# Kernel tuning notes

Measured on AMD Instinct MI355X. Metric: run time of the kernel, lower is better.

Reference implementation:

```python
import jax, jax.numpy as jnp
import numpy as np

INPUT_DIM = 64
HIDDEN_DIM = 10
OUTPUT_DIM = 5
BATCH = 4096


def setup_inputs() -> dict:
    key = jax.random.key(0)
    ks = jax.random.split(key, 11)
    s = 0.1
    return {
        "x": jax.random.normal(ks[0], (BATCH, INPUT_DIM), dtype=jnp.float32),
        # phi: Linear(1, H) -> ReLU -> Linear(H, O)
        "phi_W1": jax.random.normal(ks[1], (1, HIDDEN_DIM), dtype=jnp.float32) * s,
        "phi_b1": jax.random.normal(ks[2], (HIDDEN_DIM,), dtype=jnp.float32) * s,
        "phi_W2": jax.random.normal(ks[3], (HIDDEN_DIM, OUTPUT_DIM), dtype=jnp.float32) * s,
        "phi_b2": jax.random.normal(ks[4], (OUTPUT_DIM,), dtype=jnp.float32) * s,
        # attention: Linear(O, 1)
        "attn_W": jax.random.normal(ks[5], (OUTPUT_DIM, 1), dtype=jnp.float32) * s,
        "attn_b": jax.random.normal(ks[6], (1,), dtype=jnp.float32) * s,
        # psi: Linear(2*O, H) -> ReLU -> Linear(H, O)
        "psi_W1": jax.random.normal(ks[7], (2 * OUTPUT_DIM, HIDDEN_DIM), dtype=jnp.float32) * s,
        "psi_b1": jax.random.normal(ks[8], (HIDDEN_DIM,), dtype=jnp.float32) * s,
        "psi_W2": jax.random.normal(ks[9], (HIDDEN_DIM, OUTPUT_DIM), dtype=jnp.float32) * s,
        "psi_b2": jax.random.normal(ks[10], (OUTPUT_DIM,), dtype=jnp.float32) * s,
    }


def reference(x, phi_W1, phi_b1, phi_W2, phi_b2, attn_W, attn_b,
              psi_W1, psi_b1, psi_W2, psi_b2) -> jnp.ndarray:
    B, n = x.shape
    # phi applied per scalar feature, batched over (B, n).
    # x[:, :, None] @ phi_W1 == outer product since input dim is 1.
    h = jax.nn.relu(x[:, :, None] * phi_W1[0] + phi_b1)          # [B, n, H]
    phi_out = jnp.einsum('bnh,ho->bno', h, phi_W2) + phi_b2      # [B, n, O]
    # attention over the feature axis
    scores = jnp.einsum('bno,oa->bna', phi_out, attn_W) + attn_b  # [B, n, 1]
    weights = jax.nn.softmax(scores, axis=1)
    w = phi_out * weights                                        # [B, n, O]
    # all pairs i < j
    ii, jj = jnp.triu_indices(n, k=1)                            # [P]
    pair = jnp.concatenate([w[:, ii, :], w[:, jj, :]], axis=-1)  # [B, P, 2O]
    ph = jax.nn.relu(jnp.einsum('bpk,kh->bph', pair, psi_W1) + psi_b1)  # [B, P, H]
    psi_out = jnp.einsum('bph,ho->bpo', ph, psi_W2) + psi_b2     # [B, P, O]
    return jnp.sum(psi_out, axis=1)                              # [B, O]
```

## Files before the change

### kernel.cpp

```cpp
#include <hip/hip_runtime.h>
#include <math.h>

typedef float f2v __attribute__((ext_vector_type(2)));

#define BATCH 4096
#define NPAIRF 2016.0f

__device__ __forceinline__ f2v relu2(f2v t) {
    t.x = fmaxf(t.x, 0.0f);
    t.y = fmaxf(t.y, 0.0f);
    return t;
}

template <int CTRL>
__device__ __forceinline__ float dpp_add(float x) {
    int y = __builtin_amdgcn_update_dpp(0, __builtin_bit_cast(int, x), CTRL, 0xf, 0xf, true);
    return x + __builtin_bit_cast(float, y);
}
__device__ __forceinline__ float wave_sum63(float x) {
    x = dpp_add<0x111>(x);
    x = dpp_add<0x112>(x);
    x = dpp_add<0x114>(x);
    x = dpp_add<0x118>(x);
    x = dpp_add<0x142>(x);
    x = dpp_add<0x143>(x);
    return x;
}

__device__ __forceinline__ unsigned pack_bf16(float a, float b) {
    unsigned ua = __builtin_bit_cast(unsigned, a) + 0x8000u;
    unsigned ub = __builtin_bit_cast(unsigned, b) + 0x8000u;
    return (ua >> 16) | (ub & 0xffff0000u);
}
__device__ __forceinline__ f2v unpack_bf16(unsigned w) {
    f2v r;
    r.x = __builtin_bit_cast(float, w << 16);
    r.y = __builtin_bit_cast(float, w & 0xffff0000u);
    return r;
}

__global__ __launch_bounds__(256, 4) void akan_kernel(
    const float* __restrict__ x,
    const float* __restrict__ phi_W1, const float* __restrict__ phi_b1,
    const float* __restrict__ phi_W2, const float* __restrict__ phi_b2,
    const float* __restrict__ attn_W, const float* __restrict__ attn_b,
    const float* __restrict__ psi_W1, const float* __restrict__ psi_b1,
    const float* __restrict__ psi_W2, const float* __restrict__ psi_b2,
    float* __restrict__ out)
{
    __shared__ __align__(16) unsigned lds[4 * 640];

    const int lane = threadIdx.x & 63;
    const int wave = threadIdx.x >> 6;
    const int b = blockIdx.x * 4 + wave;
    unsigned* const lw = lds + wave * 640;

    const float xv = x[b * 64 + lane];
    float phi_out[5];
    #pragma unroll
    for (int o = 0; o < 5; ++o) phi_out[o] = phi_b2[o];
    #pragma unroll
    for (int k = 0; k < 10; ++k) {
        const float h = fmaxf(fmaf(xv, phi_W1[k], phi_b1[k]), 0.0f);
        #pragma unroll
        for (int o = 0; o < 5; ++o) phi_out[o] = fmaf(h, phi_W2[k * 5 + o], phi_out[o]);
    }

    float score = attn_b[0];
    #pragma unroll
    for (int o = 0; o < 5; ++o) score = fmaf(phi_out[o], attn_W[o], score);
    const float e = __expf(score);
    const float t63 = wave_sum63(e);
    const float ssum = __builtin_bit_cast(float,
        __builtin_amdgcn_readlane(__builtin_bit_cast(int, t63), 63));
    const float wgt = e * __builtin_amdgcn_rcpf(ssum);

    float w[5];
    #pragma unroll
    for (int o = 0; o < 5; ++o) w[o] = phi_out[o] * wgt;

    float u[10], v[10];
    #pragma unroll
    for (int hh = 0; hh < 10; ++hh) {
        float uu = psi_b1[hh];
        float vv = 0.0f;
        #pragma unroll
        for (int o = 0; o < 5; ++o) {
            uu = fmaf(w[o], psi_W1[o * 10 + hh], uu);
            vv = fmaf(w[o], psi_W1[(5 + o) * 10 + hh], vv);
        }
        u[hh] = uu; v[hh] = vv;
    }

    {
        uint4 mu, mv;
        mu.x = pack_bf16(u[0], u[1]); mu.y = pack_bf16(u[2], u[3]);
        mu.z = pack_bf16(u[4], u[5]); mu.w = pack_bf16(u[6], u[7]);
        mv.x = pack_bf16(v[0], v[1]); mv.y = pack_bf16(v[2], v[3]);
        mv.z = pack_bf16(v[4], v[5]); mv.w = pack_bf16(v[6], v[7]);
        *(uint4*)&lw[4 * lane]       = mu;
        lw[256 + lane]               = pack_bf16(u[8], u[9]);
        *(uint4*)&lw[320 + 4 * lane] = mv;
        lw[576 + lane]               = pack_bf16(v[8], v[9]);
    }

    f2v U[5], V[5], S[5];
    #pragma unroll
    for (int j = 0; j < 5; ++j) {
        U[j] = (f2v){u[2 * j], u[2 * j + 1]};
        V[j] = (f2v){v[2 * j], v[2 * j + 1]};
        S[j] = (f2v){0.0f, 0.0f};
    }

    #pragma unroll
    for (int d = 1; d <= 31; ++d) {
        const int pl = lane + d;
        const int m = pl & 63;
        const bool wrapped = pl >= 64;
        const unsigned* rb = wrapped ? lw : (lw + 320);
        const uint4 q = *(const uint4*)(rb + 4 * m);
        const unsigned c = rb[256 + m];
        const f2v R0 = unpack_bf16(q.x), R1 = unpack_bf16(q.y),
                  R2 = unpack_bf16(q.z), R3 = unpack_bf16(q.w),
                  R4 = unpack_bf16(c);
        const f2v L0 = wrapped ? V[0] : U[0];
        const f2v L1 = wrapped ? V[1] : U[1];
        const f2v L2 = wrapped ? V[2] : U[2];
        const f2v L3 = wrapped ? V[3] : U[3];
        const f2v L4 = wrapped ? V[4] : U[4];
        S[0] += relu2(L0 + R0);
        S[1] += relu2(L1 + R1);
        S[2] += relu2(L2 + R2);
        S[3] += relu2(L3 + R3);
        S[4] += relu2(L4 + R4);
    }
    if (lane < 32) {
        const int m = lane + 32;
        const unsigned* rb = lw + 320;
        const uint4 q = *(const uint4*)(rb + 4 * m);
        const unsigned c = rb[256 + m];
        S[0] += relu2(U[0] + unpack_bf16(q.x));
        S[1] += relu2(U[1] + unpack_bf16(q.y));
        S[2] += relu2(U[2] + unpack_bf16(q.z));
        S[3] += relu2(U[3] + unpack_bf16(q.w));
        S[4] += relu2(U[4] + unpack_bf16(c));
    }

    float sv[10];
    #pragma unroll
    for (int j = 0; j < 5; ++j) { sv[2 * j] = S[j].x; sv[2 * j + 1] = S[j].y; }

    float po[5];
    #pragma unroll
    for (int o = 0; o < 5; ++o) {
        float acc = 0.0f;
        #pragma unroll
        for (int hh = 0; hh < 10; ++hh)
            acc = fmaf(sv[hh], psi_W2[hh * 5 + o], acc);
        po[o] = wave_sum63(acc);
    }

    if (lane == 63) {
        #pragma unroll
        for (int o = 0; o < 5; ++o)
            out[b * 5 + o] = fmaf(NPAIRF, psi_b2[o], po[o]);
    }
}

extern "C" void kernel_launch(void* const* d_in, const int* in_sizes, int n_in,
                              void* d_out, int out_size, void* d_ws, size_t ws_size,
                              hipStream_t stream) {
    const float* x      = (const float*)d_in[0];
    const float* phi_W1 = (const float*)d_in[1];
    const float* phi_b1 = (const float*)d_in[2];
    const float* phi_W2 = (const float*)d_in[3];
    const float* phi_b2 = (const float*)d_in[4];
    const float* attn_W = (const float*)d_in[5];
    const float* attn_b = (const float*)d_in[6];
    const float* psi_W1 = (const float*)d_in[7];
    const float* psi_b1 = (const float*)d_in[8];
    const float* psi_W2 = (const float*)d_in[9];
    const float* psi_b2 = (const float*)d_in[10];
    float* outp = (float*)d_out;

    dim3 grid(BATCH / 4);
    dim3 block(256);
    akan_kernel<<<grid, block, 0, stream>>>(x, phi_W1, phi_b1, phi_W2, phi_b2,
                                            attn_W, attn_b, psi_W1, psi_b1,
                                            psi_W2, psi_b2, outp);
}
```

Baseline: 18.98 us.

## Switch pair loop to packed fp16 with fused relu-accumulate and two rows per wave

The pairwise psi hidden accumulation moves from bf16-unpacked fp32 math to packed fp16 adds. ReLU-accumulate is fused as max(S+t, S) via v_pk_max_f16, and partial sums are promoted to fp32 halfway and at the end to limit fp16 error growth. Each wave now handles two batch rows, which halves the grid and interleaves independent work to hide LDS latency. LDS is laid out in separate strided planes so no unpacking is needed. The trade-off is fp16 precision in the accumulation and higher register pressure, with launch bounds relaxed to reflect that.

```diff
diff --git a/kernel.cpp b/kernel.cpp
--- a/kernel.cpp
+++ b/kernel.cpp
@@ -2,15 +2,10 @@
 #include <math.h>
 
 typedef float f2v __attribute__((ext_vector_type(2)));
+typedef _Float16 h2 __attribute__((ext_vector_type(2)));
 
 #define BATCH 4096
 #define NPAIRF 2016.0f
-
-__device__ __forceinline__ f2v relu2(f2v t) {
-    t.x = fmaxf(t.x, 0.0f);
-    t.y = fmaxf(t.y, 0.0f);
-    return t;
-}
 
 template <int CTRL>
 __device__ __forceinline__ float dpp_add(float x) {
@@ -27,19 +22,14 @@
     return x;
 }
 
-__device__ __forceinline__ unsigned pack_bf16(float a, float b) {
-    unsigned ua = __builtin_bit_cast(unsigned, a) + 0x8000u;
-    unsigned ub = __builtin_bit_cast(unsigned, b) + 0x8000u;
-    return (ua >> 16) | (ub & 0xffff0000u);
-}
-__device__ __forceinline__ f2v unpack_bf16(unsigned w) {
-    f2v r;
-    r.x = __builtin_bit_cast(float, w << 16);
-    r.y = __builtin_bit_cast(float, w & 0xffff0000u);
+__device__ __forceinline__ h2 pkmax(h2 a, h2 b) {
+    h2 r;
+    asm("v_pk_max_f16 %0, %1, %2" : "=v"(r) : "v"(a), "v"(b));
     return r;
 }
-
-__global__ __launch_bounds__(256, 4) void akan_kernel(
+__device__ __forceinline__ h2 ash2(unsigned w) { return __builtin_bit_cast(h2, w); }
+
+__global__ __launch_bounds__(256, 2) void akan_kernel(
     const float* __restrict__ x,
     const float* __restrict__ phi_W1, const float* __restrict__ phi_b1,
     const float* __restrict__ phi_W2, const float* __restrict__ phi_b2,
@@ -48,123 +38,145 @@
     const float* __restrict__ psi_W2, const float* __restrict__ psi_b2,
     float* __restrict__ out)
 {
-    __shared__ __align__(16) unsigned lds[4 * 640];
-
+    __shared__ __align__(16) char lds[4 * 6144];
     const int lane = threadIdx.x & 63;
     const int wave = threadIdx.x >> 6;
-    const int b = blockIdx.x * 4 + wave;
-    unsigned* const lw = lds + wave * 640;
-
-    const float xv = x[b * 64 + lane];
-    float phi_out[5];
+    const int b0 = (blockIdx.x * 4 + wave) * 2;
+    char* const wslab = lds + wave * 6144;
+
+    h2 U[2][5], V[2][5], S16[2][5];
+    f2v S32[2][5];
+
     #pragma unroll
-    for (int o = 0; o < 5; ++o) phi_out[o] = phi_b2[o];
-    #pragma unroll
-    for (int k = 0; k < 10; ++k) {
-        const float h = fmaxf(fmaf(xv, phi_W1[k], phi_b1[k]), 0.0f);
-        #pragma unroll
-        for (int o = 0; o < 5; ++o) phi_out[o] = fmaf(h, phi_W2[k * 5 + o], phi_out[o]);
-    }
-
-    float score = attn_b[0];
-    #pragma unroll
-    for (int o = 0; o < 5; ++o) score = fmaf(phi_out[o], attn_W[o], score);
-    const float e = __expf(score);
-    const float t63 = wave_sum63(e);
-    const float ssum = __builtin_bit_cast(float,
-        __builtin_amdgcn_readlane(__builtin_bit_cast(int, t63), 63));
-    const float wgt = e * __builtin_amdgcn_rcpf(ssum);
-
-    float w[5];
-    #pragma unroll
-    for (int o = 0; o < 5; ++o) w[o] = phi_out[o] * wgt;
-
-    float u[10], v[10];
-    #pragma unroll
-    for (int hh = 0; hh < 10; ++hh) {
-        float uu = psi_b1[hh];
-        float vv = 0.0f;
-        #pragma unroll
-        for (int o = 0; o < 5; ++o) {
-            uu = fmaf(w[o], psi_W1[o * 10 + hh], uu);
-            vv = fmaf(w[o], psi_W1[(5 + o) * 10 + hh], vv);
-        }
-        u[hh] = uu; v[hh] = vv;
-    }
-
-    {
-        uint4 mu, mv;
-        mu.x = pack_bf16(u[0], u[1]); mu.y = pack_bf16(u[2], u[3]);
-        mu.z = pack_bf16(u[4], u[5]); mu.w = pack_bf16(u[6], u[7]);
-        mv.x = pack_bf16(v[0], v[1]); mv.y = pack_bf16(v[2], v[3]);
-        mv.z = pack_bf16(v[4], v[5]); mv.w = pack_bf16(v[6], v[7]);
-        *(uint4*)&lw[4 * lane]       = mu;
-        lw[256 + lane]               = pack_bf16(u[8], u[9]);
-        *(uint4*)&lw[320 + 4 * lane] = mv;
-        lw[576 + lane]               = pack_bf16(v[8], v[9]);
-    }
-
-    f2v U[5], V[5], S[5];
-    #pragma unroll
-    for (int j = 0; j < 5; ++j) {
-        U[j] = (f2v){u[2 * j], u[2 * j + 1]};
-        V[j] = (f2v){v[2 * j], v[2 * j + 1]};
-        S[j] = (f2v){0.0f, 0.0f};
-    }
+    for (int k = 0; k < 2; ++k) {
+        const float xv = x[(b0 + k) * 64 + lane];
+        float phi_out[5];
+        #pragma unroll
+        for (int o = 0; o < 5; ++o) phi_out[o] = phi_b2[o];
+        #pragma unroll
+        for (int kk = 0; kk < 10; ++kk) {
+            const float h = fmaxf(fmaf(xv, phi_W1[kk], phi_b1[kk]), 0.0f);
+            #pragma unroll
+            for (int o = 0; o < 5; ++o) phi_out[o] = fmaf(h, phi_W2[kk * 5 + o], phi_out[o]);
+        }
+        float score = attn_b[0];
+        #pragma unroll
+        for (int o = 0; o < 5; ++o) score = fmaf(phi_out[o], attn_W[o], score);
+        const float e = __expf(score);
+        const float t63 = wave_sum63(e);
+        const float ssum = __builtin_bit_cast(float,
+            __builtin_amdgcn_readlane(__builtin_bit_cast(int, t63), 63));
+        const float wgt = e * __builtin_amdgcn_rcpf(ssum);
+
+        float w[5];
+        #pragma unroll
+        for (int o = 0; o < 5; ++o) w[o] = phi_out[o] * wgt;
+
+        float u[10], v[10];
+        #pragma unroll
+        for (int hh = 0; hh < 10; ++hh) {
+            float uu = psi_b1[hh];
+            float vv = 0.0f;
+            #pragma unroll
+            for (int o = 0; o < 5; ++o) {
+                uu = fmaf(w[o], psi_W1[o * 10 + hh], uu);
+                vv = fmaf(w[o], psi_W1[(5 + o) * 10 + hh], vv);
+            }
+            u[hh] = uu; v[hh] = vv;
+        }
+        #pragma unroll
+        for (int j = 0; j < 5; ++j) {
+            U[k][j] = (h2){(_Float16)u[2 * j], (_Float16)u[2 * j + 1]};
+            V[k][j] = (h2){(_Float16)v[2 * j], (_Float16)v[2 * j + 1]};
+            S16[k][j] = (h2){0, 0};
+            S32[k][j] = (f2v){0.0f, 0.0f};
+        }
+        char* slab = wslab + k * 3072;
+        uint2 q;
+        q.x = __builtin_bit_cast(unsigned, U[k][0]); q.y = __builtin_bit_cast(unsigned, U[k][1]);
+        *(uint2*)(slab + lane * 8) = q;
+        q.x = __builtin_bit_cast(unsigned, U[k][2]); q.y = __builtin_bit_cast(unsigned, U[k][3]);
+        *(uint2*)(slab + 512 + lane * 8) = q;
+        *(unsigned*)(slab + 1024 + lane * 8) = __builtin_bit_cast(unsigned, U[k][4]);
+        q.x = __builtin_bit_cast(unsigned, V[k][0]); q.y = __builtin_bit_cast(unsigned, V[k][1]);
+        *(uint2*)(slab + 1536 + lane * 8) = q;
+        q.x = __builtin_bit_cast(unsigned, V[k][2]); q.y = __builtin_bit_cast(unsigned, V[k][3]);
+        *(uint2*)(slab + 2048 + lane * 8) = q;
+        *(unsigned*)(slab + 2560 + lane * 8) = __builtin_bit_cast(unsigned, V[k][4]);
+    }
+
+    const char* const rowb = wslab + lane * 8;
+
+    #define PROC(k, r0, r1, r2, r3, r4)                                  \
+        {                                                                \
+            const h2 L0 = uw ? U[k][0] : V[k][0];                        \
+            const h2 L1 = uw ? U[k][1] : V[k][1];                        \
+            const h2 L2 = uw ? U[k][2] : V[k][2];                        \
+            const h2 L3 = uw ? U[k][3] : V[k][3];                        \
+            const h2 L4 = uw ? U[k][4] : V[k][4];                        \
+            S16[k][0] = pkmax(S16[k][0] + (L0 + ash2(r0)), S16[k][0]);   \
+            S16[k][1] = pkmax(S16[k][1] + (L1 + ash2(r1)), S16[k][1]);   \
+            S16[k][2] = pkmax(S16[k][2] + (L2 + ash2(r2)), S16[k][2]);   \
+            S16[k][3] = pkmax(S16[k][3] + (L3 + ash2(r3)), S16[k][3]);   \
+            S16[k][4] = pkmax(S16[k][4] + (L4 + ash2(r4)), S16[k][4]);   \
+        }
+    #define PROMOTE()                                                    \
+        _Pragma("unroll") for (int k = 0; k < 2; ++k)                    \
+        _Pragma("unroll") for (int j = 0; j < 5; ++j) {                  \
+            S32[k][j] += (f2v){(float)S16[k][j].x, (float)S16[k][j].y};  \
+            S16[k][j] = (h2){0, 0};                                      \
+        }
 
     #pragma unroll
     for (int d = 1; d <= 31; ++d) {
-        const int pl = lane + d;
-        const int m = pl & 63;
-        const bool wrapped = pl >= 64;
-        const unsigned* rb = wrapped ? lw : (lw + 320);
-        const uint4 q = *(const uint4*)(rb + 4 * m);
-        const unsigned c = rb[256 + m];
-        const f2v R0 = unpack_bf16(q.x), R1 = unpack_bf16(q.y),
-                  R2 = unpack_bf16(q.z), R3 = unpack_bf16(q.w),
-                  R4 = unpack_bf16(c);
-        const f2v L0 = wrapped ? V[0] : U[0];
-        const f2v L1 = wrapped ? V[1] : U[1];
-        const f2v L2 = wrapped ? V[2] : U[2];
-        const f2v L3 = wrapped ? V[3] : U[3];
-        const f2v L4 = wrapped ? V[4] : U[4];
-        S[0] += relu2(L0 + R0);
-        S[1] += relu2(L1 + R1);
-        S[2] += relu2(L2 + R2);
-        S[3] += relu2(L3 + R3);
-        S[4] += relu2(L4 + R4);
+        const bool uw = lane < (64 - d);
+        const char* p = (uw ? rowb + 1536 : rowb - 512) + 8 * d;
+        const uint2    a01 = *(const uint2*)(p);
+        const uint2    a23 = *(const uint2*)(p + 512);
+        const unsigned a4  = *(const unsigned*)(p + 1024);
+        const uint2    c01 = *(const uint2*)(p + 3072);
+        const uint2    c23 = *(const uint2*)(p + 3584);
+        const unsigned c4  = *(const unsigned*)(p + 4096);
+        PROC(0, a01.x, a01.y, a23.x, a23.y, a4);
+        PROC(1, c01.x, c01.y, c23.x, c23.y, c4);
+        if (d == 16) { PROMOTE(); }
     }
     if (lane < 32) {
-        const int m = lane + 32;
-        const unsigned* rb = lw + 320;
-        const uint4 q = *(const uint4*)(rb + 4 * m);
-        const unsigned c = rb[256 + m];
-        S[0] += relu2(U[0] + unpack_bf16(q.x));
-        S[1] += relu2(U[1] + unpack_bf16(q.y));
-        S[2] += relu2(U[2] + unpack_bf16(q.z));
-        S[3] += relu2(U[3] + unpack_bf16(q.w));
-        S[4] += relu2(U[4] + unpack_bf16(c));
-    }
-
-    float sv[10];
+        const bool uw = true;
+        const char* p = rowb + 1536 + 256;
+        const uint2    a01 = *(const uint2*)(p);
+        const uint2    a23 = *(const uint2*)(p + 512);
+        const unsigned a4  = *(const unsigned*)(p + 1024);
+        const uint2    c01 = *(const uint2*)(p + 3072);
+        const uint2    c23 = *(const uint2*)(p + 3584);
+        const unsigned c4  = *(const unsigned*)(p + 4096);
+        PROC(0, a01.x, a01.y, a23.x, a23.y, a4);
+        PROC(1, c01.x, c01.y, c23.x, c23.y, c4);
+    }
+    PROMOTE();
+
     #pragma unroll
-    for (int j = 0; j < 5; ++j) { sv[2 * j] = S[j].x; sv[2 * j + 1] = S[j].y; }
-
-    float po[5];
-    #pragma unroll
-    for (int o = 0; o < 5; ++o) {
-        float acc = 0.0f;
-        #pragma unroll
-        for (int hh = 0; hh < 10; ++hh)
-            acc = fmaf(sv[hh], psi_W2[hh * 5 + o], acc);
-        po[o] = wave_sum63(acc);
-    }
-
-    if (lane == 63) {
-        #pragma unroll
-        for (int o = 0; o < 5; ++o)
-            out[b * 5 + o] = fmaf(NPAIRF, psi_b2[o], po[o]);
-    }
+    for (int k = 0; k < 2; ++k) {
+        float sv[10];
+        #pragma unroll
+        for (int j = 0; j < 5; ++j) { sv[2 * j] = S32[k][j].x; sv[2 * j + 1] = S32[k][j].y; }
+        float po[5];
+        #pragma unroll
+        for (int o = 0; o < 5; ++o) {
+            float acc = 0.0f;
+            #pragma unroll
+            for (int hh = 0; hh < 10; ++hh)
+                acc = fmaf(sv[hh], psi_W2[hh * 5 + o], acc);
+            po[o] = wave_sum63(acc);
+        }
+        if (lane == 63) {
+            #pragma unroll
+            for (int o = 0; o < 5; ++o)
+                out[(b0 + k) * 5 + o] = fmaf(NPAIRF, psi_b2[o], po[o]);
+        }
+    }
+    #undef PROC
+    #undef PROMOTE
 }
 
 extern "C" void kernel_launch(void* const* d_in, const int* in_sizes, int n_in,
@@ -183,7 +195,7 @@
     const float* psi_b2 = (const float*)d_in[10];
     float* outp = (float*)d_out;
 
-    dim3 grid(BATCH / 4);
+    dim3 grid(BATCH / 8);
     dim3 block(256);
     akan_kernel<<<grid, block, 0, stream>>>(x, phi_W1, phi_b1, phi_W2, phi_b2,
                                             attn_W, attn_b, psi_W1, psi_b1,
```

Measured after the change: 16.10 us. 15.2% less time.
